# Kernel tuning notes

Measured on AMD Instinct MI355X. Metric: run time of the kernel, lower is better.

## Reference

```python
import jax, jax.numpy as jnp
import numpy as np

B, C_IN, C_OUT, H, W, N = 2, 64, 64, 128, 128, 8
FACT = 4
H_SE = C_OUT // FACT               # 16 : SE bottleneck per direction
HID_ATTN = (N * C_OUT) // FACT     # 128: SortAttn hidden
G_ATTN = N * 2                     # 16 : SortAttn groups (group=2)
DIRECTIONS = [(1, 1), (1, -1), (-1, 1), (-1, -1), (1, 0), (-1, 0), (0, 1), (0, -1)]


def gconv1x1(x, w, groups):
    # x: [B,Cin,H,W], w: [Cout, Cin//groups] (1x1 grouped conv, no bias)
    b, cin, h, w_ = x.shape
    cout = w.shape[0]
    xg = x.reshape(b, groups, cin // groups, h * w_)
    wg = w.reshape(groups, cout // groups, cin // groups)
    y = jnp.einsum('bgip,goi->bgop', xg, wg)
    return y.reshape(b, cout, h, w_)


def channel_shuffle(x, g):
    b, c, h, w = x.shape
    return x.reshape(b, g, c // g, h, w).transpose(0, 2, 1, 3, 4).reshape(b, c, h, w)


def se2d(x, en_w, s_w, e_w, gate):
    # SE2d / SEGate2d with 1x1 en conv, n=N parallel attention branches
    y = jnp.einsum('bchw,oc->bohw', x, en_w)                      # en conv
    pooled = jnp.concatenate([y.mean((2, 3), keepdims=True),
                              y.max((2, 3), keepdims=True)], axis=1)  # [B,2C,1,1]
    hdn = jax.nn.relu(jnp.einsum('bchw,oc->bohw', pooled, s_w))   # [B,H_SE*N,1,1]
    attn = jax.nn.sigmoid(gconv1x1(hdn, e_w, N))                  # [B,N*C,1,1]
    b = y.shape[0]
    outs = y[:, None] * attn.reshape(b, N, C_OUT, 1, 1)           # [B,N,C,H,W]
    return jax.nn.sigmoid(outs) if gate else outs


def gru_dir(z, hh, h0c, d1, d2):
    # z, hh: [B,C,H,W]; h0c: [C]. Faithful to GRUDirection2d with |d| in {0,1}.
    flip_axes = tuple(ax for ax, dd in ((2, d1), (3, d2)) if dd < 0)
    if flip_axes:
        z = jnp.flip(z, flip_axes)
        hh = jnp.flip(hh, flip_axes)
    b, c, hgt, wid = z.shape
    if d1 != 0 and d2 != 0:
        # diagonal recurrence: h[i,j] = z*_h + (1-z)*h[i-1,j-1], border = h0
        init = jnp.broadcast_to(h0c[None, :, None], (b, c, wid))
        h0col = init[..., :1]

        def step(prev, zh):
            zt, ht = zh
            prev_s = jnp.concatenate([h0col, prev[..., :-1]], axis=-1)
            new = zt * ht + (1 - zt) * prev_s
            return new, new

        zm = jnp.moveaxis(z, 2, 0)
        hm = jnp.moveaxis(hh, 2, 0)
        _, out = jax.lax.scan(step, init, (zm, hm))
        out = jnp.moveaxis(out, 0, 2)
    else:
        axis = 2 if d1 != 0 else 3
        zm = jnp.moveaxis(z, axis, 0)
        hm = jnp.moveaxis(hh, axis, 0)
        init = jnp.broadcast_to(h0c[None, :, None], zm.shape[1:])

        def step(hprev, zh):
            zt, ht = zh
            new = zt * ht + (1 - zt) * hprev
            return new, new

        _, out = jax.lax.scan(step, init, (zm, hm))
        out = jnp.moveaxis(out, 0, axis)
    if flip_axes:
        out = jnp.flip(out, flip_axes)
    return out


def setup_inputs():
    key = jax.random.key(0)
    ks = jax.random.split(key, 13)
    s = 0.05
    return {
        'x': jax.random.normal(ks[0], (B, C_IN, H, W), jnp.float32),
        'h0': jax.random.normal(ks[1], (N, C_OUT), jnp.float32) * 0.1,
        'h_en_w': jax.random.normal(ks[2], (C_OUT, C_IN), jnp.float32) * s,
        'h_s_w': jax.random.normal(ks[3], (H_SE * N, 2 * C_OUT), jnp.float32) * s,
        'h_e_w': jax.random.normal(ks[4], (C_OUT * N, H_SE), jnp.float32) * s,
        'z_en_w': jax.random.normal(ks[5], (C_OUT, C_IN), jnp.float32) * s,
        'z_s_w': jax.random.normal(ks[6], (H_SE * N, 2 * C_OUT), jnp.float32) * s,
        'z_e_w': jax.random.normal(ks[7], (C_OUT * N, H_SE), jnp.float32) * s,
        'a_w1': jax.random.normal(ks[8], (HID_ATTN, (2 * N * C_OUT) // (2 * G_ATTN)), jnp.float32) * s,
        'a_w2': jax.random.normal(ks[9], (HID_ATTN, HID_ATTN // G_ATTN), jnp.float32) * s,
        'a_w3': jax.random.normal(ks[10], (HID_ATTN, HID_ATTN // G_ATTN), jnp.float32) * s,
        'a_w4': jax.random.normal(ks[11], (N * C_OUT, HID_ATTN // G_ATTN), jnp.float32) * s,
    }


def reference(x, h0, h_en_w, h_s_w, h_e_w, z_en_w, z_s_w, z_e_w, a_w1, a_w2, a_w3, a_w4):
    hhs = se2d(x, h_en_w, h_s_w, h_e_w, gate=False)   # candidate states, [B,N,C,H,W]
    zs = se2d(x, z_en_w, z_s_w, z_e_w, gate=True)     # update gates, [B,N,C,H,W]
    hs = [gru_dir(zs[:, i], hhs[:, i], h0[i], d1, d2)
          for i, (d1, d2) in enumerate(DIRECTIONS)]
    xcat = jnp.concatenate(hs, axis=1)                # [B, N*C, H, W]
    sorted_x = jnp.sort(xcat, axis=1)
    t = jnp.concatenate([xcat, sorted_x], axis=1)     # [B, 2*N*C, H, W]
    t = gconv1x1(t, a_w1, 2 * G_ATTN)
    t = channel_shuffle(t, G_ATTN)
    t = gconv1x1(t, a_w2, G_ATTN)
    t = channel_shuffle(t, G_ATTN)
    t = jax.nn.relu(gconv1x1(t, a_w3, G_ATTN))
    t = channel_shuffle(t, G_ATTN)
    scores = jax.nn.sigmoid(gconv1x1(t, a_w4, G_ATTN))
    b = xcat.shape[0]
    y = (xcat * scores).reshape(b, N, C_OUT, H, W).sum(axis=1)
    return y
```

## Files before the change

kernel.cpp:

```cpp
#include <hip/hip_runtime.h>
#include <cstdint>
#include <cstddef>

typedef unsigned int uint;
typedef unsigned short ushort;

#define DEVFN __device__ __forceinline__

DEVFN float bf2f(uint h) { return __uint_as_float(h << 16); }
DEVFN ushort f2bf(float x) {
  uint u = __float_as_uint(x);
  u = (u + 0x7FFFu + ((u >> 16) & 1u)) >> 16;
  return (ushort)u;
}
DEVFN float sigmoidf(float x) { return 1.0f / (1.0f + __expf(-x)); }

__global__ __launch_bounds__(256) void k_conv(const float* __restrict__ x,
                                              const float* __restrict__ wh,
                                              const float* __restrict__ wz,
                                              uint* __restrict__ ypack,
                                              float* __restrict__ part) {
  __shared__ __align__(16) float xt[64][66];
  __shared__ __align__(16) float wls[2][64][64];
  const int tid = threadIdx.x;
  const int b = blockIdx.x >> 8;
  const int tile = blockIdx.x & 255;
  const int pix0 = tile * 64;

  for (int idx = tid; idx < 4096; idx += 256) {
    int o = idx >> 6, c = idx & 63;
    wls[0][c][o] = wh[idx];
    wls[1][c][o] = wz[idx];
  }
  const float* xb = x + ((size_t)b << 20);
  for (int idx = tid; idx < 4096; idx += 256) {
    int c = idx >> 6, p = idx & 63;
    xt[c][p] = xb[c * 16384 + pix0 + p];
  }
  __syncthreads();

  const int p = tid & 63, og = tid >> 6, o0 = og * 16;
  float fh[16], fz[16];
#pragma unroll
  for (int j = 0; j < 16; ++j) { fh[j] = 0.0f; fz[j] = 0.0f; }

  for (int c = 0; c < 64; ++c) {
    float xv = xt[c][p];
    const float4* whp = (const float4*)&wls[0][c][o0];
    const float4* wzp = (const float4*)&wls[1][c][o0];
#pragma unroll
    for (int jj = 0; jj < 4; ++jj) {
      float4 a = whp[jj], bb = wzp[jj];
      fh[jj * 4 + 0] += xv * a.x; fh[jj * 4 + 1] += xv * a.y;
      fh[jj * 4 + 2] += xv * a.z; fh[jj * 4 + 3] += xv * a.w;
      fz[jj * 4 + 0] += xv * bb.x; fz[jj * 4 + 1] += xv * bb.y;
      fz[jj * 4 + 2] += xv * bb.z; fz[jj * 4 + 3] += xv * bb.w;
    }
  }
  uint* orow = ypack + ((size_t)(b * 16384 + pix0 + p)) * 64 + o0;
#pragma unroll
  for (int jj = 0; jj < 4; ++jj) {
    uint4 pk;
    pk.x = (uint)f2bf(fh[jj * 4 + 0]) | ((uint)f2bf(fz[jj * 4 + 0]) << 16);
    pk.y = (uint)f2bf(fh[jj * 4 + 1]) | ((uint)f2bf(fz[jj * 4 + 1]) << 16);
    pk.z = (uint)f2bf(fh[jj * 4 + 2]) | ((uint)f2bf(fz[jj * 4 + 2]) << 16);
    pk.w = (uint)f2bf(fh[jj * 4 + 3]) | ((uint)f2bf(fz[jj * 4 + 3]) << 16);
    ((uint4*)orow)[jj] = pk;
  }

  __syncthreads();
  float* xtA = &xt[0][0];
  float* ztA = &wls[0][0][0];
#pragma unroll
  for (int j = 0; j < 16; ++j) {
    xtA[(o0 + j) * 66 + p] = fh[j];
    ztA[(o0 + j) * 66 + p] = fz[j];
  }
  __syncthreads();
  if (tid < 128) {
    const int o = tid & 63;
    const float* src = (tid < 64) ? xtA : ztA;
    float sm = 0.0f, mx = -1e30f;
#pragma unroll 8
    for (int pp = 0; pp < 64; ++pp) {
      float v = src[o * 66 + pp];
      sm += v; mx = fmaxf(mx, v);
    }
    float* pb = part + ((size_t)(b * 256 + tile) * 4) * 64;
    const int st = (tid < 64) ? 0 : 2;
    pb[st * 64 + o] = sm;
    pb[(st + 1) * 64 + o] = mx;
  }
}

__global__ __launch_bounds__(256) void k_attn(const float* __restrict__ part,
                       const float* __restrict__ hsw, const float* __restrict__ zsw,
                       const float* __restrict__ hew, const float* __restrict__ zew,
                       float* __restrict__ attnb) {
  __shared__ float psum[4][64];
  __shared__ float pmax[4][64];
  __shared__ float pooled[128];
  __shared__ float hdn[128];
  const int tid = threadIdx.x;
  const int hz = blockIdx.x >> 1, bb = blockIdx.x & 1;
  const int g = tid >> 6, c = tid & 63;

  {
    float sm = 0.0f, mx = -1e30f;
    const float* pb = part + ((size_t)(bb * 256 + g * 64) * 4) * 64;
    for (int tt = 0; tt < 64; ++tt) {
      sm += pb[(size_t)tt * 256 + 2 * hz * 64 + c];
      mx = fmaxf(mx, pb[(size_t)tt * 256 + (2 * hz + 1) * 64 + c]);
    }
    psum[g][c] = sm; pmax[g][c] = mx;
  }
  __syncthreads();
  if (tid < 64) {
    float sm = psum[0][c] + psum[1][c] + psum[2][c] + psum[3][c];
    float mx = fmaxf(fmaxf(pmax[0][c], pmax[1][c]), fmaxf(pmax[2][c], pmax[3][c]));
    pooled[c] = sm * (1.0f / 16384.0f);
    pooled[64 + c] = mx;
  }
  __syncthreads();
  if (tid < 128) {
    const float* sw = hz ? zsw : hsw;
    float acc = 0.0f;
    for (int cc = 0; cc < 128; ++cc) acc += pooled[cc] * sw[tid * 128 + cc];
    hdn[tid] = fmaxf(acc, 0.0f);
  }
  __syncthreads();
  const float* ew = hz ? zew : hew;
  for (int o2 = tid; o2 < 512; o2 += 256) {
    const int gb = (o2 >> 6) * 16;
    float acc = 0.0f;
#pragma unroll
    for (int vv = 0; vv < 16; ++vv) acc += hdn[gb + vv] * ew[o2 * 16 + vv];
    attnb[(hz * 2 + bb) * 512 + o2] = sigmoidf(acc);
  }
}

__global__ __launch_bounds__(256) void k_scan(const uint* __restrict__ ypack,
                                              const float* __restrict__ attnb,
                                              const float* __restrict__ h0,
                                              ushort* __restrict__ xcat) {
  const int wid = blockIdx.x * 4 + (threadIdx.x >> 6);
  const int lane = threadIdx.x & 63;
  int i, b, s;
  if (wid < 2040) {
    i = wid / 510;
    int r = wid - i * 510;
    b = (r >= 255) ? 1 : 0;
    s = r - b * 255;
  } else {
    int w2 = wid - 2040;
    i = 4 + (w2 >> 8);
    int r = w2 & 255;
    b = r >> 7;
    s = r & 127;
  }
  int h0s, w0s, dh, dw, L;
  switch (i) {
    case 0: dh = 1;  dw = 1;
      if (s < 128) { h0s = s; w0s = 0; L = 128 - s; } else { h0s = 0; w0s = s - 127; L = 255 - s; }
      break;
    case 1: dh = 1;  dw = -1;
      if (s < 128) { h0s = 0; w0s = s; L = s + 1; } else { h0s = s - 127; w0s = 127; L = 255 - s; }
      break;
    case 2: dh = -1; dw = 1;
      if (s < 128) { h0s = s; w0s = 0; L = s + 1; } else { h0s = 127; w0s = s - 127; L = 255 - s; }
      break;
    case 3: dh = -1; dw = -1;
      if (s < 128) { h0s = 127; w0s = s; L = s + 1; } else { h0s = s - 128; w0s = 127; L = s - 127; }
      break;
    case 4: dh = 1;  dw = 0;  h0s = 0;   w0s = s; L = 128; break;
    case 5: dh = -1; dw = 0;  h0s = 127; w0s = s; L = 128; break;
    case 6: dh = 0;  dw = 1;  h0s = s;   w0s = 0; L = 128; break;
    default: dh = 0; dw = -1; h0s = s;   w0s = 127; L = 128; break;
  }
  const float ah = attnb[b * 512 + i * 64 + lane];
  const float az = attnb[1024 + b * 512 + i * 64 + lane];
  float hp = h0[i * 64 + lane];

  const int pos = b * 16384 + h0s * 128 + w0s;
  const int dstep = dh * 128 + dw;
  const uint* yp = ypack + (size_t)pos * 64 + lane;
  ushort* xp = xcat + (size_t)pos * 512 + i * 64 + lane;
  const ptrdiff_t ystep = (ptrdiff_t)dstep * 64;
  const ptrdiff_t xstep = (ptrdiff_t)dstep * 512;

#define PROC1(u) { float yh = bf2f((u) & 0xffffu), yz = bf2f((u) >> 16); \
                   float zt = sigmoidf(yz * az);                          \
                   hp = fmaf(zt, fmaf(yh, ah, -hp), hp);                  \
                   *xp = f2bf(hp); xp += xstep; }

  uint c0 = 0, c1 = 0, c2 = 0, c3 = 0, c4 = 0, c5 = 0, c6 = 0, c7 = 0;
  c0 = yp[0];
  if (1 < L) c1 = yp[ystep];
  if (2 < L) c2 = yp[2 * ystep];
  if (3 < L) c3 = yp[3 * ystep];
  if (4 < L) c4 = yp[4 * ystep];
  if (5 < L) c5 = yp[5 * ystep];
  if (6 < L) c6 = yp[6 * ystep];
  if (7 < L) c7 = yp[7 * ystep];

  for (int base = 0; base < L; base += 8) {
    uint b0 = c0, b1 = c1, b2 = c2, b3 = c3, b4 = c4, b5 = c5, b6 = c6, b7 = c7;
    const uint* ypn = yp + (ptrdiff_t)(base + 8) * ystep;
    if (base + 8 < L) {
      c0 = ypn[0];
      if (base + 9  < L) c1 = ypn[ystep];
      if (base + 10 < L) c2 = ypn[2 * ystep];
      if (base + 11 < L) c3 = ypn[3 * ystep];
      if (base + 12 < L) c4 = ypn[4 * ystep];
      if (base + 13 < L) c5 = ypn[5 * ystep];
      if (base + 14 < L) c6 = ypn[6 * ystep];
      if (base + 15 < L) c7 = ypn[7 * ystep];
    }
    PROC1(b0);
    if (base + 1 < L) PROC1(b1);
    if (base + 2 < L) PROC1(b2);
    if (base + 3 < L) PROC1(b3);
    if (base + 4 < L) PROC1(b4);
    if (base + 5 < L) PROC1(b5);
    if (base + 6 < L) PROC1(b6);
    if (base + 7 < L) PROC1(b7);
  }
#undef PROC1
}

__global__ __launch_bounds__(256, 2) void k_final(const ushort* __restrict__ xcat,
                                                  const float* __restrict__ a_w1,
                                                  const float* __restrict__ a_w2,
                                                  const float* __restrict__ a_w3,
                                                  const float* __restrict__ a_w4,
                                                  float* __restrict__ out) {
  __shared__ __align__(16) float w1s[128 * 32];
  __shared__ uint w4p[32 * 64];
  __shared__ float tb1[4][128];
  __shared__ __align__(16) float otile[16][68];

  const int tid = threadIdx.x;
  const int lane = tid & 63;
  const int wslot = tid >> 6;
  const int b = blockIdx.x >> 10;
  const int tile = blockIdx.x & 1023;
  const int pix0 = tile * 16;

  for (int idx = tid; idx < 4096; idx += 256) {
    int o = idx >> 5, ci = idx & 31;
    w1s[o * 32 + ((ci + (o >> 2)) & 31)] = a_w1[idx];
  }
  for (int idx = tid; idx < 2048; idx += 256) {
    int rk2 = idx >> 6, l = idx & 63;
    int rr = rk2 >> 2, kp = rk2 & 3;
    const float* src = a_w4 + ((l * 8 + rr) * 8 + 2 * kp);
    w4p[rk2 * 64 + l] = (uint)f2bf(src[0]) | ((uint)f2bf(src[1]) << 16);
  }

  float w2a[8], w2b[8], w3a[8], w3b[8];
  {
    const float4* p;
    p = (const float4*)(a_w2 + lane * 8);        ((float4*)w2a)[0] = p[0]; ((float4*)w2a)[1] = p[1];
    p = (const float4*)(a_w2 + 512 + lane * 8);  ((float4*)w2b)[0] = p[0]; ((float4*)w2b)[1] = p[1];
    p = (const float4*)(a_w3 + lane * 8);        ((float4*)w3a)[0] = p[0]; ((float4*)w3a)[1] = p[1];
    p = (const float4*)(a_w3 + 512 + lane * 8);  ((float4*)w3b)[0] = p[0]; ((float4*)w3b)[1] = p[1];
  }
  __syncthreads();

  const int q = lane >> 2, m4 = lane & 3;
  const int base1 = 64 * ((lane >> 3) & 1) + (lane >> 4);
  const int base3 = 64 * ((lane >> 2) & 1) + (lane >> 3);

  for (int it = 0; it < 4; ++it) {
    const int px = wslot * 4 + it;
    const int pix = pix0 + px;

    float v[8], s[8];
    {
      const uint4 pk = *(const uint4*)(xcat + (((size_t)(b * 16384 + pix)) << 9) + lane * 8);
      v[0] = bf2f(pk.x & 0xffffu); v[1] = bf2f(pk.x >> 16);
      v[2] = bf2f(pk.y & 0xffffu); v[3] = bf2f(pk.y >> 16);
      v[4] = bf2f(pk.z & 0xffffu); v[5] = bf2f(pk.z >> 16);
      v[6] = bf2f(pk.w & 0xffffu); v[7] = bf2f(pk.w >> 16);
    }
#pragma unroll
    for (int r = 0; r < 8; ++r) s[r] = v[r];

#pragma unroll
    for (int k = 2; k <= 512; k <<= 1) {
#pragma unroll
      for (int j = k >> 1; j >= 1; j >>= 1) {
        if (j >= 8) {
          const int m = j >> 3;
          const bool upper = (lane & m) != 0;
          const bool asc = (lane & (k >> 3)) == 0;
          const bool takeMin = (upper != asc);
#pragma unroll
          for (int r = 0; r < 8; ++r) {
            float o = __shfl_xor(s[r], m, 64);
            float mn = fminf(s[r], o), mx = fmaxf(s[r], o);
            s[r] = takeMin ? mn : mx;
          }
        } else if (k < 8) {
#pragma unroll
          for (int r = 0; r < 8; ++r) {
            if ((r & j) == 0) {
              int r2 = r | j;
              float mn = fminf(s[r], s[r2]), mx = fmaxf(s[r], s[r2]);
              if ((r & k) == 0) { s[r] = mn; s[r2] = mx; }
              else { s[r] = mx; s[r2] = mn; }
            }
          }
        } else {
          const bool asc = (lane & (k >> 3)) == 0;
#pragma unroll
          for (int r = 0; r < 8; ++r) {
            if ((r & j) == 0) {
              int r2 = r | j;
              float mn = fminf(s[r], s[r2]), mx = fmaxf(s[r], s[r2]);
              s[r] = asc ? mn : mx;
              s[r2] = asc ? mx : mn;
            }
          }
        }
      }
    }

    float pa[4], pb[4];
#pragma unroll
    for (int u = 0; u < 4; ++u) {
      const float* wV = &w1s[(4 * q + u) * 32];
      const float* wS = &w1s[(64 + 4 * q + u) * 32];
      float aV = 0.0f, aS = 0.0f;
#pragma unroll
      for (int r = 0; r < 8; ++r) {
        const int ci = m4 * 8 + r;
        aV += v[r] * wV[(ci + q) & 31];
        aS += s[r] * wS[(ci + q + 16) & 31];
      }
      pa[u] = aV; pb[u] = aS;
    }
#pragma unroll
    for (int u = 0; u < 4; ++u) {
      pa[u] += __shfl_xor(pa[u], 1, 64);
      pa[u] += __shfl_xor(pa[u], 2, 64);
      pb[u] += __shfl_xor(pb[u], 1, 64);
      pb[u] += __shfl_xor(pb[u], 2, 64);
    }
    const float t1a = (m4 == 0) ? pa[0] : (m4 == 1) ? pa[1] : (m4 == 2) ? pa[2] : pa[3];
    const float t1b = (m4 == 0) ? pb[0] : (m4 == 1) ? pb[1] : (m4 == 2) ? pb[2] : pb[3];

    tb1[wslot][lane] = t1a;
    tb1[wslot][64 + lane] = t1b;

    float a2 = 0.0f, b2 = 0.0f;
#pragma unroll
    for (int kk = 0; kk < 8; ++kk) {
      a2 += tb1[wslot][base1 + 8 * kk] * w2a[kk];
      b2 += tb1[wslot][base1 + 8 * kk + 4] * w2b[kk];
    }
    tb1[wslot][lane] = a2;
    tb1[wslot][64 + lane] = b2;

    float a3 = 0.0f, b3 = 0.0f;
#pragma unroll
    for (int kk = 0; kk < 8; ++kk) {
      a3 += tb1[wslot][base1 + 8 * kk] * w3a[kk];
      b3 += tb1[wslot][base1 + 8 * kk + 4] * w3b[kk];
    }
    tb1[wslot][lane] = fmaxf(a3, 0.0f);
    tb1[wslot][64 + lane] = fmaxf(b3, 0.0f);

    float in4[8];
#pragma unroll
    for (int kk = 0; kk < 8; ++kk) in4[kk] = tb1[wslot][base3 + 8 * kk];

    float prod[8];
#pragma unroll
    for (int rr = 0; rr < 8; ++rr) {
      float acc = 0.0f;
#pragma unroll
      for (int kp = 0; kp < 4; ++kp) {
        uint pw = w4p[(rr * 4 + kp) * 64 + lane];
        float wlo = __uint_as_float(pw << 16);
        float whi = __uint_as_float(pw & 0xffff0000u);
        acc += in4[2 * kp] * wlo + in4[2 * kp + 1] * whi;
      }
      prod[rr] = v[rr] * sigmoidf(acc);
    }
#pragma unroll
    for (int rr = 0; rr < 8; ++rr) {
      prod[rr] += __shfl_xor(prod[rr], 8, 64);
      prod[rr] += __shfl_xor(prod[rr], 16, 64);
      prod[rr] += __shfl_xor(prod[rr], 32, 64);
    }
    if (lane < 8) {
      float4* dst = (float4*)&otile[px][lane * 8];
      dst[0] = make_float4(prod[0], prod[1], prod[2], prod[3]);
      dst[1] = make_float4(prod[4], prod[5], prod[6], prod[7]);
    }
  }
  __syncthreads();

  for (int idx = tid; idx < 1024; idx += 256) {
    int px = idx & 15, c = idx >> 4;
    out[(((size_t)(b * 64 + c)) << 14) + pix0 + px] = otile[px][c];
  }
}

extern "C" void kernel_launch(void* const* d_in, const int* in_sizes, int n_in,
                              void* d_out, int out_size, void* d_ws, size_t ws_size,
                              hipStream_t stream) {
  const float* x      = (const float*)d_in[0];
  const float* h0     = (const float*)d_in[1];
  const float* h_en_w = (const float*)d_in[2];
  const float* h_s_w  = (const float*)d_in[3];
  const float* h_e_w  = (const float*)d_in[4];
  const float* z_en_w = (const float*)d_in[5];
  const float* z_s_w  = (const float*)d_in[6];
  const float* z_e_w  = (const float*)d_in[7];
  const float* a_w1   = (const float*)d_in[8];
  const float* a_w2   = (const float*)d_in[9];
  const float* a_w3   = (const float*)d_in[10];
  const float* a_w4   = (const float*)d_in[11];
  float* out = (float*)d_out;

  char* ws = (char*)d_ws;
  uint*   ypack = (uint*)ws;
  ushort* xcat  = (ushort*)(ws + ((size_t)8 << 20));
  float*  part  = (float*)(ws + ((size_t)40 << 20));
  float*  attnb = (float*)(ws + ((size_t)40 << 20) + (1u << 20));

  hipLaunchKernelGGL(k_conv, dim3(512), dim3(256), 0, stream, x, h_en_w, z_en_w,
                     ypack, part);
  hipLaunchKernelGGL(k_attn, dim3(4), dim3(256), 0, stream, part, h_s_w, z_s_w,
                     h_e_w, z_e_w, attnb);
  hipLaunchKernelGGL(k_scan, dim3(766), dim3(256), 0, stream, ypack, attnb, h0, xcat);
  hipLaunchKernelGGL(k_final, dim3(2048), dim3(256), 0, stream, xcat, a_w1, a_w2, a_w3,
                     a_w4, out);
}
```

Measured before the change: 264.0 us.

## Sort packed bf16 keys with v_pk_min/max_u16 and raise k_final occupancy

```diff
diff --git a/kernel.cpp b/kernel.cpp
--- a/kernel.cpp
+++ b/kernel.cpp
@@ -14,6 +14,14 @@
   return (ushort)u;
 }
 DEVFN float sigmoidf(float x) { return 1.0f / (1.0f + __expf(-x)); }
+
+DEVFN uint pkminu(uint a, uint b) {
+  uint r; asm("v_pk_min_u16 %0, %1, %2" : "=v"(r) : "v"(a), "v"(b)); return r;
+}
+DEVFN uint pkmaxu(uint a, uint b) {
+  uint r; asm("v_pk_max_u16 %0, %1, %2" : "=v"(r) : "v"(a), "v"(b)); return r;
+}
+DEVFN uint ror16(uint x) { return (x >> 16) | (x << 16); }
 
 __global__ __launch_bounds__(256) void k_conv(const float* __restrict__ x,
                                               const float* __restrict__ wh,
@@ -228,7 +236,7 @@
 #undef PROC1
 }
 
-__global__ __launch_bounds__(256, 2) void k_final(const ushort* __restrict__ xcat,
+__global__ __launch_bounds__(256, 3) void k_final(const ushort* __restrict__ xcat,
                                                   const float* __restrict__ a_w1,
                                                   const float* __restrict__ a_w2,
                                                   const float* __restrict__ a_w3,
@@ -257,13 +265,11 @@
     w4p[rk2 * 64 + l] = (uint)f2bf(src[0]) | ((uint)f2bf(src[1]) << 16);
   }
 
-  float w2a[8], w2b[8], w3a[8], w3b[8];
-  {
-    const float4* p;
-    p = (const float4*)(a_w2 + lane * 8);        ((float4*)w2a)[0] = p[0]; ((float4*)w2a)[1] = p[1];
-    p = (const float4*)(a_w2 + 512 + lane * 8);  ((float4*)w2b)[0] = p[0]; ((float4*)w2b)[1] = p[1];
-    p = (const float4*)(a_w3 + lane * 8);        ((float4*)w3a)[0] = p[0]; ((float4*)w3a)[1] = p[1];
-    p = (const float4*)(a_w3 + 512 + lane * 8);  ((float4*)w3b)[0] = p[0]; ((float4*)w3b)[1] = p[1];
+  uint w2p[8], w3p[8];
+#pragma unroll
+  for (int kk = 0; kk < 8; ++kk) {
+    w2p[kk] = (uint)f2bf(a_w2[lane * 8 + kk]) | ((uint)f2bf(a_w2[512 + lane * 8 + kk]) << 16);
+    w3p[kk] = (uint)f2bf(a_w3[lane * 8 + kk]) | ((uint)f2bf(a_w3[512 + lane * 8 + kk]) << 16);
   }
   __syncthreads();
 
@@ -275,55 +281,87 @@
     const int px = wslot * 4 + it;
     const int pix = pix0 + px;
 
-    float v[8], s[8];
+    uint vp[4], s[4];
     {
       const uint4 pk = *(const uint4*)(xcat + (((size_t)(b * 16384 + pix)) << 9) + lane * 8);
-      v[0] = bf2f(pk.x & 0xffffu); v[1] = bf2f(pk.x >> 16);
-      v[2] = bf2f(pk.y & 0xffffu); v[3] = bf2f(pk.y >> 16);
-      v[4] = bf2f(pk.z & 0xffffu); v[5] = bf2f(pk.z >> 16);
-      v[6] = bf2f(pk.w & 0xffffu); v[7] = bf2f(pk.w >> 16);
-    }
-#pragma unroll
-    for (int r = 0; r < 8; ++r) s[r] = v[r];
+      vp[0] = pk.x; vp[1] = pk.y; vp[2] = pk.z; vp[3] = pk.w;
+    }
+#pragma unroll
+    for (int p = 0; p < 4; ++p) {
+      uint sgn = (vp[p] >> 15) & 0x00010001u;
+      s[p] = vp[p] ^ (0x80008000u | (sgn * 0x7FFFu));
+    }
 
 #pragma unroll
     for (int k = 2; k <= 512; k <<= 1) {
 #pragma unroll
-      for (int j = k >> 1; j >= 1; j >>= 1) {
-        if (j >= 8) {
-          const int m = j >> 3;
-          const bool upper = (lane & m) != 0;
-          const bool asc = (lane & (k >> 3)) == 0;
-          const bool takeMin = (upper != asc);
-#pragma unroll
-          for (int r = 0; r < 8; ++r) {
-            float o = __shfl_xor(s[r], m, 64);
-            float mn = fminf(s[r], o), mx = fmaxf(s[r], o);
-            s[r] = takeMin ? mn : mx;
-          }
-        } else if (k < 8) {
-#pragma unroll
-          for (int r = 0; r < 8; ++r) {
-            if ((r & j) == 0) {
-              int r2 = r | j;
-              float mn = fminf(s[r], s[r2]), mx = fmaxf(s[r], s[r2]);
-              if ((r & k) == 0) { s[r] = mn; s[r2] = mx; }
-              else { s[r] = mx; s[r2] = mn; }
-            }
-          }
-        } else {
-          const bool asc = (lane & (k >> 3)) == 0;
-#pragma unroll
-          for (int r = 0; r < 8; ++r) {
-            if ((r & j) == 0) {
-              int r2 = r | j;
-              float mn = fminf(s[r], s[r2]), mx = fmaxf(s[r], s[r2]);
-              s[r] = asc ? mn : mx;
-              s[r2] = asc ? mx : mn;
-            }
-          }
+      for (int j = k >> 1; j >= 8; j >>= 1) {
+        const int m = j >> 3;
+        const bool asc = (lane & (k >> 3)) == 0;
+        const bool takeMin = ((lane & m) != 0) != asc;
+#pragma unroll
+        for (int p = 0; p < 4; ++p) {
+          uint o = __shfl_xor(s[p], m, 64);
+          uint mn = pkminu(s[p], o), mx = pkmaxu(s[p], o);
+          s[p] = takeMin ? mn : mx;
         }
       }
+      if (k >= 8) {
+        const bool asc = (lane & (k >> 3)) == 0;
+        uint mn0 = pkminu(s[0], s[2]), mx0 = pkmaxu(s[0], s[2]);
+        uint mn1 = pkminu(s[1], s[3]), mx1 = pkmaxu(s[1], s[3]);
+        s[0] = asc ? mn0 : mx0;  s[2] = asc ? mx0 : mn0;
+        s[1] = asc ? mn1 : mx1;  s[3] = asc ? mx1 : mn1;
+      }
+      if (k >= 8) {
+        const bool asc = (lane & (k >> 3)) == 0;
+        uint mn0 = pkminu(s[0], s[1]), mx0 = pkmaxu(s[0], s[1]);
+        uint mn1 = pkminu(s[2], s[3]), mx1 = pkmaxu(s[2], s[3]);
+        s[0] = asc ? mn0 : mx0;  s[1] = asc ? mx0 : mn0;
+        s[2] = asc ? mn1 : mx1;  s[3] = asc ? mx1 : mn1;
+      } else if (k == 4) {
+        uint mn0 = pkminu(s[0], s[1]), mx0 = pkmaxu(s[0], s[1]);
+        uint mn1 = pkminu(s[2], s[3]), mx1 = pkmaxu(s[2], s[3]);
+        s[0] = mn0; s[1] = mx0;
+        s[2] = mx1; s[3] = mn1;
+      }
+      if (k >= 8) {
+        const bool asc = (lane & (k >> 3)) == 0;
+#pragma unroll
+        for (int p = 0; p < 4; ++p) {
+          uint t = ror16(s[p]);
+          uint mn = pkminu(s[p], t), mx = pkmaxu(s[p], t);
+          uint ra = (mn & 0x0000FFFFu) | (mx & 0xFFFF0000u);
+          s[p] = asc ? ra : ror16(ra);
+        }
+      } else if (k == 4) {
+#pragma unroll
+        for (int p = 0; p < 4; ++p) {
+          uint t = ror16(s[p]);
+          uint mn = pkminu(s[p], t), mx = pkmaxu(s[p], t);
+          uint ra = (mn & 0x0000FFFFu) | (mx & 0xFFFF0000u);
+          s[p] = (p < 2) ? ra : ror16(ra);
+        }
+      } else {
+#pragma unroll
+        for (int p = 0; p < 4; ++p) {
+          uint t = ror16(s[p]);
+          uint mn = pkminu(s[p], t), mx = pkmaxu(s[p], t);
+          uint ra = (mn & 0x0000FFFFu) | (mx & 0xFFFF0000u);
+          s[p] = ((p & 1) == 0) ? ra : ror16(ra);
+        }
+      }
+    }
+
+    float vf[8], sf[8];
+#pragma unroll
+    for (int p = 0; p < 4; ++p) {
+      uint ns = ((~s[p]) >> 15) & 0x00010001u;
+      uint sb = s[p] ^ (0x80008000u | (ns * 0x7FFFu));
+      sf[2 * p]     = __uint_as_float(sb << 16);
+      sf[2 * p + 1] = __uint_as_float(sb & 0xFFFF0000u);
+      vf[2 * p]     = __uint_as_float(vp[p] << 16);
+      vf[2 * p + 1] = __uint_as_float(vp[p] & 0xFFFF0000u);
     }
 
     float pa[4], pb[4];
@@ -335,8 +373,8 @@
 #pragma unroll
       for (int r = 0; r < 8; ++r) {
         const int ci = m4 * 8 + r;
-        aV += v[r] * wV[(ci + q) & 31];
-        aS += s[r] * wS[(ci + q + 16) & 31];
+        aV += vf[r] * wV[(ci + q) & 31];
+        aS += sf[r] * wS[(ci + q + 16) & 31];
       }
       pa[u] = aV; pb[u] = aS;
     }
@@ -356,8 +394,10 @@
     float a2 = 0.0f, b2 = 0.0f;
 #pragma unroll
     for (int kk = 0; kk < 8; ++kk) {
-      a2 += tb1[wslot][base1 + 8 * kk] * w2a[kk];
-      b2 += tb1[wslot][base1 + 8 * kk + 4] * w2b[kk];
+      float wa = __uint_as_float(w2p[kk] << 16);
+      float wb = __uint_as_float(w2p[kk] & 0xFFFF0000u);
+      a2 += tb1[wslot][base1 + 8 * kk] * wa;
+      b2 += tb1[wslot][base1 + 8 * kk + 4] * wb;
     }
     tb1[wslot][lane] = a2;
     tb1[wslot][64 + lane] = b2;
@@ -365,8 +405,10 @@
     float a3 = 0.0f, b3 = 0.0f;
 #pragma unroll
     for (int kk = 0; kk < 8; ++kk) {
-      a3 += tb1[wslot][base1 + 8 * kk] * w3a[kk];
-      b3 += tb1[wslot][base1 + 8 * kk + 4] * w3b[kk];
+      float wa = __uint_as_float(w3p[kk] << 16);
+      float wb = __uint_as_float(w3p[kk] & 0xFFFF0000u);
+      a3 += tb1[wslot][base1 + 8 * kk] * wa;
+      b3 += tb1[wslot][base1 + 8 * kk + 4] * wb;
     }
     tb1[wslot][lane] = fmaxf(a3, 0.0f);
     tb1[wslot][64 + lane] = fmaxf(b3, 0.0f);
@@ -386,7 +428,7 @@
         float whi = __uint_as_float(pw & 0xffff0000u);
         acc += in4[2 * kp] * wlo + in4[2 * kp + 1] * whi;
       }
-      prod[rr] = v[rr] * sigmoidf(acc);
+      prod[rr] = vf[rr] * sigmoidf(acc);
     }
 #pragma unroll
     for (int rr = 0; rr < 8; ++rr) {
```

New measurement: 222.4 us. -15.8%, faster.
